# Kernel optimization log

Hardware: AMD Instinct MI355X
Metric: run time of the kernel (lower is better)

Reference implementation:

```python
import jax, jax.numpy as jnp
import numpy as np

B, S, D, H, R, N, KR = 2, 2048, 1024, 16, 256, 8, 128
DH = D // H
EPS = 1e-5


def setup_inputs() -> dict:
    key = jax.random.key(0)
    ks = jax.random.split(key, 20)
    sm = lambda k, n: jax.nn.softmax(jax.random.normal(k, (B, S, n), jnp.float32), axis=-1)
    return {
        "x": jax.random.normal(ks[0], (B, S, D), jnp.float32),
        "fqk_w_Q": sm(ks[1], N),
        "fqk_w_K": sm(ks[2], N),
        "fv_w": sm(ks[3], N),
        "rqk_w_Q": sm(ks[4], N),
        "rqk_w_K": sm(ks[5], N),
        "rv_w": sm(ks[6], N),
        "feature_know_w": sm(ks[7], N),
        "restore_know_w": sm(ks[8], N),
        "f_qk": jax.random.normal(ks[9], (N, D, R), jnp.float32) * 0.02,
        "f_v": jax.random.normal(ks[10], (N, D, R), jnp.float32) * 0.02,
        "r_qk": jax.random.normal(ks[11], (N, R, D), jnp.float32) * 0.02,
        "r_v": jax.random.normal(ks[12], (N, R, D), jnp.float32) * 0.02,
        "f_know": jax.random.normal(ks[13], (N, D, KR), jnp.float32) * 0.02,
        "r_know": jax.random.normal(ks[14], (N, KR, D), jnp.float32) * 0.02,
        "W_O": jax.random.normal(ks[15], (D, D), jnp.float32) * 0.02,
        "ln1_g": jnp.ones((D,), jnp.float32),
        "ln1_b": jnp.zeros((D,), jnp.float32),
        "ln2_g": jnp.ones((D,), jnp.float32),
        "ln2_b": jnp.zeros((D,), jnp.float32),
    }


def _layernorm(x, g, b):
    m = jnp.mean(x, axis=-1, keepdims=True)
    v = jnp.mean(jnp.square(x - m), axis=-1, keepdims=True)
    return (x - m) * jax.lax.rsqrt(v + EPS) * g + b


def _feature(x, neurons, w):
    # fused form of einsum('bsd,ndr->bsnr') + einsum('bsnr,bsn->bsr')
    return jnp.einsum('bsd,bsn,ndr->bsr', x, w, neurons)


def _restore(h, neurons, w):
    # fused form of einsum('bsr,nrd->bsnd') + einsum('bsnd,bsn->bsd')
    return jnp.einsum('bsr,bsn,nrd->bsd', h, w, neurons)


def _causal_sdpa(q, k, v):
    # q,k,v: [B,H,S,DH]
    scores = jnp.einsum('bhqd,bhkd->bhqk', q, k) / jnp.sqrt(jnp.float32(DH))
    mask = jnp.tril(jnp.ones((S, S), bool))
    scores = jnp.where(mask, scores, jnp.finfo(scores.dtype).min)
    p = jax.nn.softmax(scores, axis=-1)
    return jnp.einsum('bhqk,bhkd->bhqd', p, v)


def _block(x, fqk_w_Q, fqk_w_K, fv_w, rqk_w_Q, rqk_w_K, rv_w,
           feature_know_w, restore_know_w, f_qk, f_v, r_qk, r_v,
           f_know, r_know, W_O, ln1_g, ln1_b, ln2_g, ln2_b):
    nx = _layernorm(x, ln1_g, ln1_b)
    h_q = _feature(nx, f_qk, fqk_w_Q)
    h_k = _feature(nx, f_qk, fqk_w_K)
    h_v = _feature(nx, f_v, fv_w)
    Q = _restore(h_q, r_qk, rqk_w_Q)
    K = _restore(h_k, r_qk, rqk_w_K)
    V = _restore(h_v, r_v, rv_w)
    to_heads = lambda t: t.reshape(B, S, H, DH).transpose(0, 2, 1, 3)
    attn = _causal_sdpa(to_heads(Q), to_heads(K), to_heads(V))
    attn = attn.transpose(0, 2, 1, 3).reshape(B, S, D)
    attn_out = attn @ W_O.T  # nn.Linear(d_model,d_model,bias=False)
    x = x + attn_out
    nx2 = _layernorm(x, ln2_g, ln2_b)
    h = _feature(nx2, f_know, feature_know_w)
    know_out = _restore(h, r_know, restore_know_w)
    return x + know_out


def reference(x, fqk_w_Q, fqk_w_K, fv_w, rqk_w_Q, rqk_w_K, rv_w,
              feature_know_w, restore_know_w, f_qk, f_v, r_qk, r_v,
              f_know, r_know, W_O, ln1_g, ln1_b, ln2_g, ln2_b):
    return _block(x, fqk_w_Q, fqk_w_K, fv_w, rqk_w_Q, rqk_w_K, rv_w,
                  feature_know_w, restore_know_w, f_qk, f_v, r_qk, r_v,
                  f_know, r_know, W_O, ln1_g, ln1_b, ln2_g, ln2_b)
```

## Files before the change

### kernel.cpp

```cpp
#include <hip/hip_runtime.h>
#include <hip/hip_bf16.h>


typedef __bf16 bf16_t;
typedef __bf16 bf16x4 __attribute__((ext_vector_type(4)));
typedef __bf16 bf16x8 __attribute__((ext_vector_type(8)));
typedef float f32x4 __attribute__((ext_vector_type(4)));

#define B_DIM 2
#define S_LEN 2048
#define D_DIM 1024
#define H_NUM 16
#define DH 64
#define N_NEU 8
#define R_DIM 256
#define KR_DIM 128
#define ROWS (B_DIM * S_LEN)

static __device__ __forceinline__ void gl_lds16(const void* g, void* l)
{
    __builtin_amdgcn_global_load_lds(
        (__attribute__((address_space(1))) void*)(g),
        (__attribute__((address_space(3))) void*)(l), 16, 0, 0);
}
// ... 78 lines not shown

__global__ __launch_bounds__(256)
void ln2x_kernel(const float* __restrict__ x, const bf16_t* __restrict__ P0,
                 const bf16_t* __restrict__ P1, const float* __restrict__ g,
                 const float* __restrict__ beta, float* __restrict__ outf,
                 bf16_t* __restrict__ outn)
{
    __shared__ float red[4];
    const int row = blockIdx.x;
    const int tid = threadIdx.x;
    const size_t base = (size_t)row * D_DIM + tid * 4;
    float4 v  = *(const float4*)&x[base];
    bf16x4 p0 = *(const bf16x4*)&P0[base];
    bf16x4 p1 = *(const bf16x4*)&P1[base];
    v.x += (float)p0[0] + (float)p1[0];
    v.y += (float)p0[1] + (float)p1[1];
    v.z += (float)p0[2] + (float)p1[2];
    v.w += (float)p0[3] + (float)p1[3];
    *(float4*)&outf[base] = v;

    float s = v.x + v.y + v.z + v.w;
#pragma unroll
    for (int o = 32; o; o >>= 1) s += __shfl_down(s, o);
    if ((tid & 63) == 0) red[tid >> 6] = s;
    __syncthreads();
    float mean = (red[0] + red[1] + red[2] + red[3]) * (1.f / D_DIM);
    __syncthreads();

    float dx = v.x - mean, dy = v.y - mean, dz = v.z - mean, dw = v.w - mean;
    float q = dx * dx + dy * dy + dz * dz + dw * dw;
#pragma unroll
    for (int o = 32; o; o >>= 1) q += __shfl_down(q, o);
    if ((tid & 63) == 0) red[tid >> 6] = q;
    __syncthreads();
    float var = (red[0] + red[1] + red[2] + red[3]) * (1.f / D_DIM);
    float rstd = rsqrtf(var + 1e-5f);

    float4 gv = *(const float4*)&g[tid * 4];
    float4 bv = *(const float4*)&beta[tid * 4];
    bf16_t* op = outn + base;
    op[0] = (bf16_t)(dx * rstd * gv.x + bv.x);
    op[1] = (bf16_t)(dy * rstd * gv.y + bv.y);
    op[2] = (bf16_t)(dz * rstd * gv.z + bv.z);
    op[3] = (bf16_t)(dw * rstd * gv.w + bv.w);
}

__global__ __launch_bounds__(256)
void wsf_kernel(const bf16_t* __restrict__ y,
                const float* __restrict__ wfQ, const float* __restrict__ wrQ,
                const float* __restrict__ wfK, const float* __restrict__ wrK,
                const float* __restrict__ wfV, const float* __restrict__ wrV,
                bf16_t* __restrict__ sq, bf16_t* __restrict__ sk, bf16_t* __restrict__ sv)
{
    const int r = threadIdx.x;
    const int row = blockIdx.x;
    const bf16_t* yrow = y + (size_t)row * 4096;
    const float* fQ = wfQ + row * N_NEU;
    const float* fK = wfK + row * N_NEU;
    const float* fV = wfV + row * N_NEU;
    float aQ = 0.f, aK = 0.f, aV = 0.f;
#pragma unroll
    for (int n = 0; n < N_NEU; n++) {
        float yq = (float)yrow[n * R_DIM + r];
        float yv = (float)yrow[2048 + n * R_DIM + r];
        aQ += fQ[n] * yq;
        aK += fK[n] * yq;
        aV += fV[n] * yv;
    }
    const float* rQ = wrQ + row * N_NEU;
    const float* rK = wrK + row * N_NEU;
    const float* rV = wrV + row * N_NEU;
    const size_t rb = (size_t)row * 2048;
#pragma unroll
    for (int n = 0; n < N_NEU; n++) {
        sq[rb + n * R_DIM + r] = (bf16_t)(rQ[n] * aQ);
        sk[rb + n * R_DIM + r] = (bf16_t)(rK[n] * aK);
        sv[rb + n * R_DIM + r] = (bf16_t)(rV[n] * aV);
    }
}

__global__ __launch_bounds__(256)
void ws2_kernel(const bf16_t* __restrict__ P0, const bf16_t* __restrict__ P1,
                const float* __restrict__ wf, const float* __restrict__ wr,
                bf16_t* __restrict__ sout)
{
    const int lr = threadIdx.x >> 7;
    const int r  = threadIdx.x & 127;
    const int row = blockIdx.x * 2 + lr;
    const size_t rb = (size_t)row * (N_NEU * KR_DIM);
    const float* wfp = wf + row * N_NEU;
    const float* wrp = wr + row * N_NEU;
    float acc = 0.f;
#pragma unroll
    for (int n = 0; n < N_NEU; n++) {
        size_t i = rb + n * KR_DIM + r;
        acc += wfp[n] * ((float)P0[i] + (float)P1[i]);
    }
    bf16_t* srow = sout + rb;
#pragma unroll
    for (int n = 0; n < N_NEU; n++) srow[n * KR_DIM + r] = (bf16_t)(wrp[n] * acc);
}

template<int EPI>
__global__ __launch_bounds__(512, 2)
void gemm256_kernel(const bf16_t* __restrict__ A, const bf16_t* __restrict__ Bt,
                    const bf16_t* __restrict__ Bt2, int splitMy,
                    void* Cout, int M, int N, int K)
{
    __shared__ bf16_t As[3][256][32];
    __shared__ bf16_t Bs[3][128][32];
    const int tid = threadIdx.x;
    const int l = tid & 63, w = tid >> 6;
    const int wr = w >> 1, wc = w & 1;

    const int nbxy = gridDim.x * gridDim.y;
    int bid = blockIdx.y * gridDim.x + blockIdx.x;
    if ((nbxy & 7) == 0) bid = (bid & 7) * (nbxy >> 3) + (bid >> 3);
    const int bx = bid % gridDim.x, by = bid / gridDim.x;

    const int m0 = by * 256, n0 = bx * 128;
    const bf16_t* Bsel = (by < splitMy) ? Bt : Bt2;

    int kbeg = 0, kend = K;
    if constexpr (EPI == 2) { const int half = K >> 1; kbeg = blockIdx.z * half; kend = kbeg + half; }

    const int strow  = w * 16 + (l >> 2);
    const int scelem = ((((l & 3) * 16) ^ ((strow & 6) << 3)) >> 1);
    const bf16_t* Ag0 = A    + (size_t)(m0 + strow) * K + scelem;
    const bf16_t* Ag1 = A    + (size_t)(m0 + strow + 128) * K + scelem;
    const bf16_t* Bg0 = Bsel + (size_t)(n0 + strow) * K + scelem;

    auto stage = [&](int buf, int k0) {
        char* dA = (char*)&As[buf][0][0] + w * 1024;
        char* dB = (char*)&Bs[buf][0][0] + w * 1024;
        gl_lds16(Ag0 + k0, dA);
        gl_lds16(Ag1 + k0, dA + 8192);
        gl_lds16(Bg0 + k0, dB);
    };

    f32x4 acc[4][4];
    const f32x4 zero = {0.f, 0.f, 0.f, 0.f};
#pragma unroll
    for (int i = 0; i < 4; i++)
#pragma unroll
        for (int j = 0; j < 4; j++) acc[i][j] = zero;

    const int fr  = l & 15;
    const int fkb = (l >> 4) * 16;

    stage(0, kbeg);
    stage(1, kbeg + 32);

    const int nK = (kend - kbeg) >> 5;
// ... 21 lines not shown
            bv[i] = *(const bf16x8*)(Bb + rowB * 64 + (fkb ^ ((rowB & 6) << 3)));
        }

        if (it + 2 < nK) stage((it + 2) % 3, kbeg + (it + 2) * 32);

        __builtin_amdgcn_s_setprio(1);
#pragma unroll
        for (int mi = 0; mi < 4; mi++)
#pragma unroll
            for (int ni = 0; ni < 4; ni++)
                acc[mi][ni] = __builtin_amdgcn_mfma_f32_16x16x32_bf16(af[mi], bv[ni], acc[mi][ni], 0, 0, 0);
        __builtin_amdgcn_s_setprio(0);
    }

    const int orow = (l >> 4) * 4;
    const int ocol = l & 15;
#pragma unroll
    for (int mi = 0; mi < 4; mi++)
#pragma unroll
        for (int ni = 0; ni < 4; ni++)
#pragma unroll
            for (int j = 0; j < 4; j++) {
                int row = m0 + wr * 64 + mi * 16 + orow + j;
                int col = n0 + wc * 64 + ni * 16 + ocol;
                size_t idx = (size_t)row * N + col;
                if constexpr (EPI == 0) {
                    ((bf16_t*)Cout)[idx] = (bf16_t)acc[mi][ni][j];
                } else {
                    ((bf16_t*)Cout)[(size_t)blockIdx.z * M * N + idx] = (bf16_t)acc[mi][ni][j];
                }
            }
}

template<int EPI>
__global__ __launch_bounds__(256)
void gemm_kernel(const bf16_t* __restrict__ A, const bf16_t* __restrict__ Bt,
                 const bf16_t* __restrict__ Bt2, int splitMy,
                 void* Cout, const float* resid, int M, int N, int K)
{
    __shared__ bf16_t As[3][128][32];
    __shared__ bf16_t Bs[3][128][32];
    const int tid = threadIdx.x;
    const int l = tid & 63, w = tid >> 6;
    const int wr = w >> 1, wc = w & 1;

    const int nbxy = gridDim.x * gridDim.y;
    int bid = blockIdx.y * gridDim.x + blockIdx.x;
    if ((nbxy & 7) == 0) bid = (bid & 7) * (nbxy >> 3) + (bid >> 3);
    const int bx = bid % gridDim.x, by = bid / gridDim.x;

    const int m0 = by * 128, n0 = bx * 128;
    const bf16_t* Bsel = (by < splitMy) ? Bt : Bt2;

    int kbeg = 0, kend = K;

    const int srow = l >> 2;
    const int scolswz = (((l & 3) * 16) ^ ((srow & 6) << 3)) >> 1;
    const bf16_t* Ag0 = A    + (size_t)(m0 + w * 32 + srow) * K + scolswz;
    const bf16_t* Ag1 = Ag0 + (size_t)16 * K;
    const bf16_t* Bg0 = Bsel + (size_t)(n0 + w * 32 + srow) * K + scolswz;
    const bf16_t* Bg1 = Bg0 + (size_t)16 * K;

    auto stage = [&](int buf, int k0) {
        char* Asb = (char*)&As[buf][0][0] + w * 2048;
        char* Bsb = (char*)&Bs[buf][0][0] + w * 2048;
        gl_lds16(Ag0 + k0, Asb);
        gl_lds16(Ag1 + k0, Asb + 1024);
        gl_lds16(Bg0 + k0, Bsb);
        gl_lds16(Bg1 + k0, Bsb + 1024);
    };

    f32x4 acc[4][4];
    const f32x4 zero = {0.f, 0.f, 0.f, 0.f};
#pragma unroll
    for (int i = 0; i < 4; i++)
#pragma unroll
        for (int j = 0; j < 4; j++) acc[i][j] = zero;

    const int fr = l & 15;
    const int fkb = (l >> 4) * 16;

    stage(0, kbeg);
    stage(1, kbeg + 32);

    const int nK = (kend - kbeg) >> 5;
    for (int it = 0; it < nK; ++it) {
        if (it + 1 < nK) {
            asm volatile("s_waitcnt vmcnt(4)" ::: "memory");
        } else {
            asm volatile("s_waitcnt vmcnt(0)" ::: "memory");
        }
        __builtin_amdgcn_s_barrier();
        __builtin_amdgcn_sched_barrier(0);

        const int cur = it % 3;
        const char* Ab = (const char*)&As[cur][0][0];
        const char* Bb = (const char*)&Bs[cur][0][0];
        bf16x8 af[4], bv[4];
#pragma unroll
        for (int i = 0; i < 4; i++) {
            const int rowA = wr * 64 + i * 16 + fr;
            af[i] = *(const bf16x8*)(Ab + rowA * 64 + (fkb ^ ((rowA & 6) << 3)));
        }
#pragma unroll
        for (int i = 0; i < 4; i++) {
            const int rowB = wc * 64 + i * 16 + fr;
            bv[i] = *(const bf16x8*)(Bb + rowB * 64 + (fkb ^ ((rowB & 6) << 3)));
        }

        if (it + 2 < nK) stage((it + 2) % 3, kbeg + (it + 2) * 32);

        __builtin_amdgcn_s_setprio(1);
#pragma unroll
        for (int mi = 0; mi < 4; mi++)
#pragma unroll
            for (int ni = 0; ni < 4; ni++)
                acc[mi][ni] = __builtin_amdgcn_mfma_f32_16x16x32_bf16(af[mi], bv[ni], acc[mi][ni], 0, 0, 0);
        __builtin_amdgcn_s_setprio(0);
    }

    const int orow = (l >> 4) * 4;
    const int ocol = l & 15;
#pragma unroll
    for (int mi = 0; mi < 4; mi++)
#pragma unroll
        for (int ni = 0; ni < 4; ni++)
#pragma unroll
            for (int j = 0; j < 4; j++) {
                int row = m0 + wr * 64 + mi * 16 + orow + j;
                int col = n0 + wc * 64 + ni * 16 + ocol;
                size_t idx = (size_t)row * N + col;
                ((float*)Cout)[idx] = acc[mi][ni][j] + resid[idx];
            }
}

__global__ __launch_bounds__(256)
void fa_kernel(const bf16_t* __restrict__ Q, const bf16_t* __restrict__ K,
               const bf16_t* __restrict__ Vt, bf16_t* __restrict__ O)
{
    __shared__ bf16_t Ks[128][72];
    __shared__ bf16_t Vs[64][136];
    __shared__ bf16_t Ps[4][16][136];

    const int tid = threadIdx.x;
    const int l = tid & 63, w = tid >> 6;

    const int bid  = blockIdx.x;
    const int xcd  = bid & 7;
    const int slot = bid >> 3;
    const int head = slot & 3;
    const int jq   = slot >> 2;
    const int bh   = xcd * 4 + head;
    const int b = bh >> 4, h = bh & 15;

    const bf16_t* Qp = Q + (size_t)b * S_LEN * D_DIM + h * DH;
    const bf16_t* Kp = K + (size_t)b * S_LEN * D_DIM + h * DH;
    const bf16_t* Vp = Vt + (size_t)b * D_DIM * S_LEN + (size_t)h * DH * S_LEN;

    const int fr = l & 15, fg = l >> 4, fk = fg * 8;
    const int srow = tid >> 2;
    const int scol = (tid & 3) * 16;
    const bf16_t* Kst = Kp + (size_t)srow * D_DIM + scol;
    const bf16_t* Vst = Vp + (size_t)srow * S_LEN + scol;

    bf16x8 ones8;
#pragma unroll
    for (int i = 0; i < 8; i++) ones8[i] = (bf16_t)1.f;

    const f32x4 zero = {0.f, 0.f, 0.f, 0.f};
    const float C_LOG2 = 0.125f * 1.44269504f;

    for (int pass = 0; pass < 2; ++pass) {
        const int qb = pass ? jq : (31 - jq);
        const int q0 = qb * 64;
        const int nt = (qb >> 1) + 1;

        bf16x8 qf[2];
#pragma unroll
        for (int ks = 0; ks < 2; ks++)
            qf[ks] = *(const bf16x8*)(Qp + (size_t)(q0 + w * 16 + fr) * D_DIM + ks * 32 + fk);

        f32x4 o[4];
        f32x4 la = zero;
        float m_r[4];
#pragma unroll
        for (int j = 0; j < 4; j++) { o[j] = zero; m_r[j] = -1e30f; }

        uint4 kva = *(const uint4*)(Kst);
        uint4 kvb = *(const uint4*)(Kst + 8);
        uint4 kvc = *(const uint4*)(Kst + (size_t)64 * D_DIM);
        uint4 kvd = *(const uint4*)(Kst + (size_t)64 * D_DIM + 8);
        uint4 vva = *(const uint4*)(Vst);
        uint4 vvb = *(const uint4*)(Vst + 8);
        uint4 vvc = *(const uint4*)(Vst + 64);
        uint4 vvd = *(const uint4*)(Vst + 72);

        for (int t = 0; t < nt; t++) {
            const int k0 = t * 128;
            __syncthreads();
            *(uint4*)&Ks[srow][scol]          = kva;
            *(uint4*)&Ks[srow][scol + 8]      = kvb;
            *(uint4*)&Ks[64 + srow][scol]     = kvc;
            *(uint4*)&Ks[64 + srow][scol + 8] = kvd;
            *(uint4*)&Vs[srow][scol]          = vva;
            *(uint4*)&Vs[srow][scol + 8]      = vvb;
            *(uint4*)&Vs[srow][64 + scol]     = vvc;
            *(uint4*)&Vs[srow][64 + scol + 8] = vvd;
            __syncthreads();

            if (t + 1 < nt) {
                const int kn = k0 + 128;
                kva = *(const uint4*)(Kst + (size_t)kn * D_DIM);
                kvb = *(const uint4*)(Kst + (size_t)kn * D_DIM + 8);
                kvc = *(const uint4*)(Kst + (size_t)(kn + 64) * D_DIM);
                kvd = *(const uint4*)(Kst + (size_t)(kn + 64) * D_DIM + 8);
                vva = *(const uint4*)(Vst + kn);
                vvb = *(const uint4*)(Vst + kn + 8);
                vvc = *(const uint4*)(Vst + kn + 64);
                vvd = *(const uint4*)(Vst + kn + 72);
            }

            f32x4 sc[2][4];
#pragma unroll
            for (int s2 = 0; s2 < 2; s2++)
#pragma unroll
                for (int ni = 0; ni < 4; ni++) sc[s2][ni] = zero;
            __builtin_amdgcn_s_setprio(1);
#pragma unroll
            for (int ks = 0; ks < 2; ks++) {
#pragma unroll
                for (int s2 = 0; s2 < 2; s2++)
#pragma unroll
                    for (int ni = 0; ni < 4; ni++) {
                        bf16x8 kf = *(const bf16x8*)&Ks[s2 * 64 + ni * 16 + fr][ks * 32 + fk];
                        sc[s2][ni] = __builtin_amdgcn_mfma_f32_16x16x32_bf16(qf[ks], kf, sc[s2][ni], 0, 0, 0);
                    }
            }
            __builtin_amdgcn_s_setprio(0);

            float p[2][4][4];
            if (t == nt - 1) {
#pragma unroll
                for (int s2 = 0; s2 < 2; s2++)
#pragma unroll
                    for (int ni = 0; ni < 4; ni++) {
                        const int key = k0 + s2 * 64 + ni * 16 + fr;
#pragma unroll
                        for (int j = 0; j < 4; j++) {
                            const int qg = q0 + w * 16 + fg * 4 + j;
                            p[s2][ni][j] = (key <= qg) ? sc[s2][ni][j] * C_LOG2 : -1e30f;
                        }
                    }
            } else {
#pragma unroll
                for (int s2 = 0; s2 < 2; s2++)
#pragma unroll
                    for (int ni = 0; ni < 4; ni++)
#pragma unroll
                        for (int j = 0; j < 4; j++)
                            p[s2][ni][j] = sc[s2][ni][j] * C_LOG2;
            }

#pragma unroll
            for (int j = 0; j < 4; j++) {
                float rmax = p[0][0][j];
#pragma unroll
                for (int s2 = 0; s2 < 2; s2++)
#pragma unroll
                    for (int ni = 0; ni < 4; ni++) rmax = fmaxf(rmax, p[s2][ni][j]);
#pragma unroll
                for (int d = 1; d < 16; d <<= 1) rmax = fmaxf(rmax, __shfl_xor(rmax, d));
                if (rmax > m_r[j] + 8.f) {
                    float scale = exp2f(m_r[j] - rmax);
                    la[j] *= scale;
#pragma unroll
                    for (int nc = 0; nc < 4; nc++) o[nc][j] *= scale;
                    m_r[j] = rmax;
                }
#pragma unroll
                for (int s2 = 0; s2 < 2; s2++)
#pragma unroll
                    for (int ni = 0; ni < 4; ni++)
                        p[s2][ni][j] = exp2f(p[s2][ni][j] - m_r[j]);
            }

#pragma unroll
            for (int s2 = 0; s2 < 2; s2++)
#pragma unroll
                for (int ni = 0; ni < 4; ni++)
#pragma unroll
                    for (int j = 0; j < 4; j++)
                        Ps[w][fg * 4 + j][s2 * 64 + ni * 16 + fr] = (bf16_t)p[s2][ni][j];

            __builtin_amdgcn_s_setprio(1);
#pragma unroll
            for (int ks = 0; ks < 4; ks++) {
                bf16x8 pa = *(const bf16x8*)&Ps[w][fr][ks * 32 + fk];
                la = __builtin_amdgcn_mfma_f32_16x16x32_bf16(pa, ones8, la, 0, 0, 0);
#pragma unroll
                for (int nc = 0; nc < 4; nc++) {
                    bf16x8 vf = *(const bf16x8*)&Vs[nc * 16 + fr][ks * 32 + fk];
                    o[nc] = __builtin_amdgcn_mfma_f32_16x16x32_bf16(pa, vf, o[nc], 0, 0, 0);
                }
            }
            __builtin_amdgcn_s_setprio(0);
        }

#pragma unroll
        for (int j = 0; j < 4; j++) {
            const float inv = 1.f / la[j];
            const int q = q0 + w * 16 + fg * 4 + j;
            bf16_t* op = O + (size_t)(b * S_LEN + q) * D_DIM + h * DH;
#pragma unroll
            for (int nc = 0; nc < 4; nc++)
                op[nc * 16 + fr] = (bf16_t)(o[nc][j] * inv);
        }
    }
}

extern "C" void kernel_launch(void* const* d_in, const int* in_sizes, int n_in,
                              void* d_out, int out_size, void* d_ws, size_t ws_size,
                              hipStream_t stream)
{
    const float* x      = (const float*)d_in[0];
    const float* fqk_wQ = (const float*)d_in[1];
    const float* fqk_wK = (const float*)d_in[2];
    const float* fv_w   = (const float*)d_in[3];
    const float* rqk_wQ = (const float*)d_in[4];
    const float* rqk_wK = (const float*)d_in[5];
    const float* rv_w   = (const float*)d_in[6];
    const float* fkn_w  = (const float*)d_in[7];
    const float* rkn_w  = (const float*)d_in[8];
    const float* f_qk   = (const float*)d_in[9];
    const float* f_v    = (const float*)d_in[10];
    const float* r_qk   = (const float*)d_in[11];
    const float* r_v    = (const float*)d_in[12];
    const float* f_know = (const float*)d_in[13];
    const float* r_know = (const float*)d_in[14];
    const float* W_O    = (const float*)d_in[15];
    const float* ln1g   = (const float*)d_in[16];
    const float* ln1b   = (const float*)d_in[17];
    const float* ln2g   = (const float*)d_in[18];
    const float* ln2b   = (const float*)d_in[19];
    float* out_f = (float*)d_out;
    (void)ws_size; (void)in_sizes; (void)n_in; (void)out_size;

    char* ws = (char*)d_ws;
    const size_t MB = 1024 * 1024;
    bf16_t* rqkT   = (bf16_t*)(ws + 0 * MB);
    bf16_t* rvT    = (bf16_t*)(ws + 4 * MB);
    bf16_t* rknT   = (bf16_t*)(ws + 8 * MB);
    bf16_t* woB    = (bf16_t*)(ws + 10 * MB);
    bf16_t* fknT   = (bf16_t*)(ws + 12 * MB);
    bf16_t* buf_nx = (bf16_t*)(ws + 14 * MB);
    bf16_t* buf_y  = (bf16_t*)(ws + 22 * MB);
    char*   buf_s  = ws + 54 * MB;
    bf16_t* fqkT   = (bf16_t*)(buf_s);
    bf16_t* fvT    = (bf16_t*)(buf_s + 4 * MB);
    bf16_t* s_q    = (bf16_t*)(buf_s);
    bf16_t* s_k    = (bf16_t*)(buf_s) + (size_t)4096 * 2048;
    bf16_t* s_v    = (bf16_t*)(buf_s) + (size_t)8192 * 2048;
    bf16_t* attn   = (bf16_t*)(buf_s);
    bf16_t* P0     = (bf16_t*)(buf_s + 16 * MB);
    bf16_t* P0k    = (bf16_t*)(buf_s);
    bf16_t* sk2    = (bf16_t*)(buf_s + 32 * MB);
    bf16_t* Qb     = buf_y;
    bf16_t* Kb     = buf_y + (size_t)4096 * 1024;
    bf16_t* Vb     = buf_y + (size_t)8192 * 1024;
    bf16_t* Vt     = buf_nx;

    const dim3 blk256(256), blk512(512), blkT(32, 8);

    tcast_kernel<<<dim3(R_DIM / 32, D_DIM / 32, N_NEU), blkT, 0, stream>>>(f_qk, fqkT, D_DIM, R_DIM);
    tcast_kernel<<<dim3(R_DIM / 32, D_DIM / 32, N_NEU), blkT, 0, stream>>>(f_v, fvT, D_DIM, R_DIM);
    tcast_kernel<<<dim3(KR_DIM / 32, D_DIM / 32, N_NEU), blkT, 0, stream>>>(f_know, fknT, D_DIM, KR_DIM);
    tcast_kernel<<<dim3(D_DIM / 32, 2048 / 32, 1), blkT, 0, stream>>>(r_qk, rqkT, 2048, D_DIM);
    tcast_kernel<<<dim3(D_DIM / 32, 2048 / 32, 1), blkT, 0, stream>>>(r_v, rvT, 2048, D_DIM);
    tcast_kernel<<<dim3(D_DIM / 32, 1024 / 32, 1), blkT, 0, stream>>>(r_know, rknT, 1024, D_DIM);
    cast_kernel<<<dim3(1024 * 1024 / 4 / 256), blk256, 0, stream>>>(W_O, woB, 1024 * 1024 / 4);

    ln_kernel<<<dim3(ROWS), blk256, 0, stream>>>(x, ln1g, ln1b, buf_nx);

    gemm256_kernel<0><<<dim3(32, 16), blk512, 0, stream>>>(buf_nx, fqkT, fqkT, 1 << 30, buf_y, 4096, 4096, 1024);

    wsf_kernel<<<dim3(ROWS), blk256, 0, stream>>>(buf_y, fqk_wQ, rqk_wQ, fqk_wK, rqk_wK, fv_w, rv_w, s_q, s_k, s_v);

    gemm256_kernel<0><<<dim3(8, 48), blk512, 0, stream>>>((bf16_t*)buf_s, rqkT, rvT, 32, buf_y, 12288, 1024, 2048);

    tbf_kernel<<<dim3(D_DIM / 32, S_LEN / 32, B_DIM), blkT, 0, stream>>>(Vb, Vt, S_LEN, D_DIM);

    fa_kernel<<<dim3(512), blk256, 0, stream>>>(Qb, Kb, Vt, attn);

    gemm256_kernel<2><<<dim3(8, 16, 2), blk512, 0, stream>>>(attn, woB, woB, 1 << 30, P0, 4096, 1024, 1024);

    ln2x_kernel<<<dim3(ROWS), blk256, 0, stream>>>(x, P0, P0 + (size_t)4096 * 1024, ln2g, ln2b, out_f, buf_nx);

    gemm256_kernel<2><<<dim3(8, 16, 2), blk512, 0, stream>>>(buf_nx, fknT, fknT, 1 << 30, P0k, 4096, 1024, 1024);

    ws2_kernel<<<dim3(ROWS / 2), blk256, 0, stream>>>(P0k, P0k + (size_t)4096 * 1024, fkn_w, rkn_w, sk2);

    gemm_kernel<1><<<dim3(8, 32), blk256, 0, stream>>>(sk2, rknT, rknT, 1 << 30, d_out, out_f, 4096, 1024, 1024);
}
```

Measured before the change: 290.7 us.

## Vectorize gating kernels and split flash attention into one q-block per workgroup

The wsf and ws2 gating kernels now give each thread 8 contiguous bf16 elements with 128-bit loads and stores, handling several rows per block. This cuts per-element memory instructions and the number of tiny blocks. The flash-attention kernel no longer pairs two q-blocks per workgroup; it launches 1024 workgroups, each taking one q-block in a zig-zag order so that heavy and light causal tiles interleave across the grid. That gives finer parallelism and load balance, at the cost of relying on the hardware scheduler to even out the causal imbalance.

```diff
diff --git a/kernel.cpp b/kernel.cpp
--- a/kernel.cpp
+++ b/kernel.cpp
@@ -154,30 +154,45 @@
                 const float* __restrict__ wfV, const float* __restrict__ wrV,
                 bf16_t* __restrict__ sq, bf16_t* __restrict__ sk, bf16_t* __restrict__ sv)
 {
-    const int r = threadIdx.x;
-    const int row = blockIdx.x;
+    const int lr = threadIdx.x >> 5;
+    const int rc = (threadIdx.x & 31) * 8;
+    const int row = blockIdx.x * 8 + lr;
     const bf16_t* yrow = y + (size_t)row * 4096;
     const float* fQ = wfQ + row * N_NEU;
     const float* fK = wfK + row * N_NEU;
     const float* fV = wfV + row * N_NEU;
-    float aQ = 0.f, aK = 0.f, aV = 0.f;
+
+    float aQ[8], aK[8], aV[8];
+#pragma unroll
+    for (int i = 0; i < 8; i++) { aQ[i] = 0.f; aK[i] = 0.f; aV[i] = 0.f; }
 #pragma unroll
     for (int n = 0; n < N_NEU; n++) {
-        float yq = (float)yrow[n * R_DIM + r];
-        float yv = (float)yrow[2048 + n * R_DIM + r];
-        aQ += fQ[n] * yq;
-        aK += fK[n] * yq;
-        aV += fV[n] * yv;
+        bf16x8 vq = *(const bf16x8*)(yrow + n * R_DIM + rc);
+        bf16x8 vv = *(const bf16x8*)(yrow + 2048 + n * R_DIM + rc);
+        const float cQ = fQ[n], cK = fK[n], cV = fV[n];
+#pragma unroll
+        for (int i = 0; i < 8; i++) {
+            float q = (float)vq[i], v = (float)vv[i];
+            aQ[i] += cQ * q; aK[i] += cK * q; aV[i] += cV * v;
+        }
     }
     const float* rQ = wrQ + row * N_NEU;
     const float* rK = wrK + row * N_NEU;
     const float* rV = wrV + row * N_NEU;
-    const size_t rb = (size_t)row * 2048;
+    const size_t rb = (size_t)row * 2048 + rc;
 #pragma unroll
     for (int n = 0; n < N_NEU; n++) {
-        sq[rb + n * R_DIM + r] = (bf16_t)(rQ[n] * aQ);
-        sk[rb + n * R_DIM + r] = (bf16_t)(rK[n] * aK);
-        sv[rb + n * R_DIM + r] = (bf16_t)(rV[n] * aV);
+        bf16x8 oq, ok, ov;
+        const float cQ = rQ[n], cK = rK[n], cV = rV[n];
+#pragma unroll
+        for (int i = 0; i < 8; i++) {
+            oq[i] = (bf16_t)(cQ * aQ[i]);
+            ok[i] = (bf16_t)(cK * aK[i]);
+            ov[i] = (bf16_t)(cV * aV[i]);
+        }
+        *(bf16x8*)(sq + rb + n * R_DIM) = oq;
+        *(bf16x8*)(sk + rb + n * R_DIM) = ok;
+        *(bf16x8*)(sv + rb + n * R_DIM) = ov;
     }
 }
 
@@ -186,21 +201,32 @@
                 const float* __restrict__ wf, const float* __restrict__ wr,
                 bf16_t* __restrict__ sout)
 {
-    const int lr = threadIdx.x >> 7;
-    const int r  = threadIdx.x & 127;
-    const int row = blockIdx.x * 2 + lr;
-    const size_t rb = (size_t)row * (N_NEU * KR_DIM);
+    const int lr = threadIdx.x >> 4;
+    const int rc = (threadIdx.x & 15) * 8;
+    const int row = blockIdx.x * 16 + lr;
+    const size_t rb = (size_t)row * (N_NEU * KR_DIM) + rc;
     const float* wfp = wf + row * N_NEU;
     const float* wrp = wr + row * N_NEU;
-    float acc = 0.f;
+
+    float acc[8];
+#pragma unroll
+    for (int i = 0; i < 8; i++) acc[i] = 0.f;
 #pragma unroll
     for (int n = 0; n < N_NEU; n++) {
-        size_t i = rb + n * KR_DIM + r;
-        acc += wfp[n] * ((float)P0[i] + (float)P1[i]);
-    }
-    bf16_t* srow = sout + rb;
-#pragma unroll
-    for (int n = 0; n < N_NEU; n++) srow[n * KR_DIM + r] = (bf16_t)(wrp[n] * acc);
+        bf16x8 p0 = *(const bf16x8*)(P0 + rb + n * KR_DIM);
+        bf16x8 p1 = *(const bf16x8*)(P1 + rb + n * KR_DIM);
+        const float c = wfp[n];
+#pragma unroll
+        for (int i = 0; i < 8; i++) acc[i] += c * ((float)p0[i] + (float)p1[i]);
+    }
+#pragma unroll
+    for (int n = 0; n < N_NEU; n++) {
+        bf16x8 o;
+        const float c = wrp[n];
+#pragma unroll
+        for (int i = 0; i < 8; i++) o[i] = (bf16_t)(c * acc[i]);
+        *(bf16x8*)(sout + rb + n * KR_DIM) = o;
+    }
 }
 
 template<int EPI>
@@ -425,9 +451,13 @@
     const int xcd  = bid & 7;
     const int slot = bid >> 3;
     const int head = slot & 3;
-    const int jq   = slot >> 2;
+    const int j5   = slot >> 2;
+    const int t5   = j5 & 7, u5 = j5 >> 3;
+    const int qb   = 8 * u5 + ((u5 & 1) ? (7 - t5) : t5);
     const int bh   = xcd * 4 + head;
     const int b = bh >> 4, h = bh & 15;
+    const int q0 = qb * 64;
+    const int nt = (qb >> 1) + 1;
 
     const bf16_t* Qp = Q + (size_t)b * S_LEN * D_DIM + h * DH;
     const bf16_t* Kp = K + (size_t)b * S_LEN * D_DIM + h * DH;
@@ -446,151 +476,145 @@
     const f32x4 zero = {0.f, 0.f, 0.f, 0.f};
     const float C_LOG2 = 0.125f * 1.44269504f;
 
-    for (int pass = 0; pass < 2; ++pass) {
-        const int qb = pass ? jq : (31 - jq);
-        const int q0 = qb * 64;
-        const int nt = (qb >> 1) + 1;
-
-        bf16x8 qf[2];
-#pragma unroll
-        for (int ks = 0; ks < 2; ks++)
-            qf[ks] = *(const bf16x8*)(Qp + (size_t)(q0 + w * 16 + fr) * D_DIM + ks * 32 + fk);
-
-        f32x4 o[4];
-        f32x4 la = zero;
-        float m_r[4];
-#pragma unroll
-        for (int j = 0; j < 4; j++) { o[j] = zero; m_r[j] = -1e30f; }
-
-        uint4 kva = *(const uint4*)(Kst);
-        uint4 kvb = *(const uint4*)(Kst + 8);
-        uint4 kvc = *(const uint4*)(Kst + (size_t)64 * D_DIM);
-        uint4 kvd = *(const uint4*)(Kst + (size_t)64 * D_DIM + 8);
-        uint4 vva = *(const uint4*)(Vst);
-        uint4 vvb = *(const uint4*)(Vst + 8);
-        uint4 vvc = *(const uint4*)(Vst + 64);
-        uint4 vvd = *(const uint4*)(Vst + 72);
-
-        for (int t = 0; t < nt; t++) {
-            const int k0 = t * 128;
-            __syncthreads();
-            *(uint4*)&Ks[srow][scol]          = kva;
-            *(uint4*)&Ks[srow][scol + 8]      = kvb;
-            *(uint4*)&Ks[64 + srow][scol]     = kvc;
-            *(uint4*)&Ks[64 + srow][scol + 8] = kvd;
-            *(uint4*)&Vs[srow][scol]          = vva;
-            *(uint4*)&Vs[srow][scol + 8]      = vvb;
-            *(uint4*)&Vs[srow][64 + scol]     = vvc;
-            *(uint4*)&Vs[srow][64 + scol + 8] = vvd;
-            __syncthreads();
-
-            if (t + 1 < nt) {
-                const int kn = k0 + 128;
-                kva = *(const uint4*)(Kst + (size_t)kn * D_DIM);
-                kvb = *(const uint4*)(Kst + (size_t)kn * D_DIM + 8);
-                kvc = *(const uint4*)(Kst + (size_t)(kn + 64) * D_DIM);
-                kvd = *(const uint4*)(Kst + (size_t)(kn + 64) * D_DIM + 8);
-                vva = *(const uint4*)(Vst + kn);
-                vvb = *(const uint4*)(Vst + kn + 8);
-                vvc = *(const uint4*)(Vst + kn + 64);
-                vvd = *(const uint4*)(Vst + kn + 72);
+    bf16x8 qf[2];
+#pragma unroll
+    for (int ks = 0; ks < 2; ks++)
+        qf[ks] = *(const bf16x8*)(Qp + (size_t)(q0 + w * 16 + fr) * D_DIM + ks * 32 + fk);
+
+    f32x4 o[4];
+    f32x4 la = zero;
+    float m_r[4];
+#pragma unroll
+    for (int j = 0; j < 4; j++) { o[j] = zero; m_r[j] = -1e30f; }
+
+    uint4 kva = *(const uint4*)(Kst);
+    uint4 kvb = *(const uint4*)(Kst + 8);
+    uint4 kvc = *(const uint4*)(Kst + (size_t)64 * D_DIM);
+    uint4 kvd = *(const uint4*)(Kst + (size_t)64 * D_DIM + 8);
+    uint4 vva = *(const uint4*)(Vst);
+    uint4 vvb = *(const uint4*)(Vst + 8);
+    uint4 vvc = *(const uint4*)(Vst + 64);
+    uint4 vvd = *(const uint4*)(Vst + 72);
+
+    for (int t = 0; t < nt; t++) {
+        const int k0 = t * 128;
+        __syncthreads();
+        *(uint4*)&Ks[srow][scol]          = kva;
+        *(uint4*)&Ks[srow][scol + 8]      = kvb;
+        *(uint4*)&Ks[64 + srow][scol]     = kvc;
+        *(uint4*)&Ks[64 + srow][scol + 8] = kvd;
+        *(uint4*)&Vs[srow][scol]          = vva;
+        *(uint4*)&Vs[srow][scol + 8]      = vvb;
+        *(uint4*)&Vs[srow][64 + scol]     = vvc;
+        *(uint4*)&Vs[srow][64 + scol + 8] = vvd;
+        __syncthreads();
+
+        if (t + 1 < nt) {
+            const int kn = k0 + 128;
+            kva = *(const uint4*)(Kst + (size_t)kn * D_DIM);
+            kvb = *(const uint4*)(Kst + (size_t)kn * D_DIM + 8);
+            kvc = *(const uint4*)(Kst + (size_t)(kn + 64) * D_DIM);
+            kvd = *(const uint4*)(Kst + (size_t)(kn + 64) * D_DIM + 8);
+            vva = *(const uint4*)(Vst + kn);
+            vvb = *(const uint4*)(Vst + kn + 8);
+            vvc = *(const uint4*)(Vst + kn + 64);
+            vvd = *(const uint4*)(Vst + kn + 72);
+        }
+
+        f32x4 sc[2][4];
+#pragma unroll
+        for (int s2 = 0; s2 < 2; s2++)
+#pragma unroll
+            for (int ni = 0; ni < 4; ni++) sc[s2][ni] = zero;
+        __builtin_amdgcn_s_setprio(1);
+#pragma unroll
+        for (int ks = 0; ks < 2; ks++) {
+#pragma unroll
+            for (int s2 = 0; s2 < 2; s2++)
+#pragma unroll
+                for (int ni = 0; ni < 4; ni++) {
+                    bf16x8 kf = *(const bf16x8*)&Ks[s2 * 64 + ni * 16 + fr][ks * 32 + fk];
+                    sc[s2][ni] = __builtin_amdgcn_mfma_f32_16x16x32_bf16(qf[ks], kf, sc[s2][ni], 0, 0, 0);
+                }
+        }
+        __builtin_amdgcn_s_setprio(0);
+
+        float p[2][4][4];
+        if (t == nt - 1) {
+#pragma unroll
+            for (int s2 = 0; s2 < 2; s2++)
+#pragma unroll
+                for (int ni = 0; ni < 4; ni++) {
+                    const int key = k0 + s2 * 64 + ni * 16 + fr;
+#pragma unroll
+                    for (int j = 0; j < 4; j++) {
+                        const int qg = q0 + w * 16 + fg * 4 + j;
+                        p[s2][ni][j] = (key <= qg) ? sc[s2][ni][j] * C_LOG2 : -1e30f;
+                    }
+                }
+        } else {
+#pragma unroll
+            for (int s2 = 0; s2 < 2; s2++)
+#pragma unroll
+                for (int ni = 0; ni < 4; ni++)
+#pragma unroll
+                    for (int j = 0; j < 4; j++)
+                        p[s2][ni][j] = sc[s2][ni][j] * C_LOG2;
+        }
+
+#pragma unroll
+        for (int j = 0; j < 4; j++) {
+            float rmax = p[0][0][j];
+#pragma unroll
+            for (int s2 = 0; s2 < 2; s2++)
+#pragma unroll
+                for (int ni = 0; ni < 4; ni++) rmax = fmaxf(rmax, p[s2][ni][j]);
+#pragma unroll
+            for (int d = 1; d < 16; d <<= 1) rmax = fmaxf(rmax, __shfl_xor(rmax, d));
+            if (rmax > m_r[j] + 8.f) {
+                float scale = exp2f(m_r[j] - rmax);
+                la[j] *= scale;
+#pragma unroll
+                for (int nc = 0; nc < 4; nc++) o[nc][j] *= scale;
+                m_r[j] = rmax;
             }
-
-            f32x4 sc[2][4];
 #pragma unroll
             for (int s2 = 0; s2 < 2; s2++)
 #pragma unroll
-                for (int ni = 0; ni < 4; ni++) sc[s2][ni] = zero;
-            __builtin_amdgcn_s_setprio(1);
-#pragma unroll
-            for (int ks = 0; ks < 2; ks++) {
-#pragma unroll
-                for (int s2 = 0; s2 < 2; s2++)
-#pragma unroll
-                    for (int ni = 0; ni < 4; ni++) {
-                        bf16x8 kf = *(const bf16x8*)&Ks[s2 * 64 + ni * 16 + fr][ks * 32 + fk];
-                        sc[s2][ni] = __builtin_amdgcn_mfma_f32_16x16x32_bf16(qf[ks], kf, sc[s2][ni], 0, 0, 0);
-                    }
+                for (int ni = 0; ni < 4; ni++)
+                    p[s2][ni][j] = exp2f(p[s2][ni][j] - m_r[j]);
+        }
+
+#pragma unroll
+        for (int s2 = 0; s2 < 2; s2++)
+#pragma unroll
+            for (int ni = 0; ni < 4; ni++)
+#pragma unroll
+                for (int j = 0; j < 4; j++)
+                    Ps[w][fg * 4 + j][s2 * 64 + ni * 16 + fr] = (bf16_t)p[s2][ni][j];
+
+        __builtin_amdgcn_s_setprio(1);
+#pragma unroll
+        for (int ks = 0; ks < 4; ks++) {
+            bf16x8 pa = *(const bf16x8*)&Ps[w][fr][ks * 32 + fk];
+            la = __builtin_amdgcn_mfma_f32_16x16x32_bf16(pa, ones8, la, 0, 0, 0);
+#pragma unroll
+            for (int nc = 0; nc < 4; nc++) {
+                bf16x8 vf = *(const bf16x8*)&Vs[nc * 16 + fr][ks * 32 + fk];
+                o[nc] = __builtin_amdgcn_mfma_f32_16x16x32_bf16(pa, vf, o[nc], 0, 0, 0);
             }
-            __builtin_amdgcn_s_setprio(0);
-
-            float p[2][4][4];
-            if (t == nt - 1) {
-#pragma unroll
-                for (int s2 = 0; s2 < 2; s2++)
-#pragma unroll
-                    for (int ni = 0; ni < 4; ni++) {
-                        const int key = k0 + s2 * 64 + ni * 16 + fr;
-#pragma unroll
-                        for (int j = 0; j < 4; j++) {
-                            const int qg = q0 + w * 16 + fg * 4 + j;
-                            p[s2][ni][j] = (key <= qg) ? sc[s2][ni][j] * C_LOG2 : -1e30f;
-                        }
-                    }
-            } else {
-#pragma unroll
-                for (int s2 = 0; s2 < 2; s2++)
-#pragma unroll
-                    for (int ni = 0; ni < 4; ni++)
-#pragma unroll
-                        for (int j = 0; j < 4; j++)
-                            p[s2][ni][j] = sc[s2][ni][j] * C_LOG2;
-            }
-
-#pragma unroll
-            for (int j = 0; j < 4; j++) {
-                float rmax = p[0][0][j];
-#pragma unroll
-                for (int s2 = 0; s2 < 2; s2++)
-#pragma unroll
-                    for (int ni = 0; ni < 4; ni++) rmax = fmaxf(rmax, p[s2][ni][j]);
-#pragma unroll
-                for (int d = 1; d < 16; d <<= 1) rmax = fmaxf(rmax, __shfl_xor(rmax, d));
-                if (rmax > m_r[j] + 8.f) {
-                    float scale = exp2f(m_r[j] - rmax);
-                    la[j] *= scale;
-#pragma unroll
-                    for (int nc = 0; nc < 4; nc++) o[nc][j] *= scale;
-                    m_r[j] = rmax;
-                }
-#pragma unroll
-                for (int s2 = 0; s2 < 2; s2++)
-#pragma unroll
-                    for (int ni = 0; ni < 4; ni++)
-                        p[s2][ni][j] = exp2f(p[s2][ni][j] - m_r[j]);
-            }
-
-#pragma unroll
-            for (int s2 = 0; s2 < 2; s2++)
-#pragma unroll
-                for (int ni = 0; ni < 4; ni++)
-#pragma unroll
-                    for (int j = 0; j < 4; j++)
-                        Ps[w][fg * 4 + j][s2 * 64 + ni * 16 + fr] = (bf16_t)p[s2][ni][j];
-
-            __builtin_amdgcn_s_setprio(1);
-#pragma unroll
-            for (int ks = 0; ks < 4; ks++) {
-                bf16x8 pa = *(const bf16x8*)&Ps[w][fr][ks * 32 + fk];
-                la = __builtin_amdgcn_mfma_f32_16x16x32_bf16(pa, ones8, la, 0, 0, 0);
-#pragma unroll
-                for (int nc = 0; nc < 4; nc++) {
-                    bf16x8 vf = *(const bf16x8*)&Vs[nc * 16 + fr][ks * 32 + fk];
-                    o[nc] = __builtin_amdgcn_mfma_f32_16x16x32_bf16(pa, vf, o[nc], 0, 0, 0);
-                }
-            }
-            __builtin_amdgcn_s_setprio(0);
-        }
-
-#pragma unroll
-        for (int j = 0; j < 4; j++) {
-            const float inv = 1.f / la[j];
-            const int q = q0 + w * 16 + fg * 4 + j;
-            bf16_t* op = O + (size_t)(b * S_LEN + q) * D_DIM + h * DH;
-#pragma unroll
-            for (int nc = 0; nc < 4; nc++)
-                op[nc * 16 + fr] = (bf16_t)(o[nc][j] * inv);
-        }
+        }
+        __builtin_amdgcn_s_setprio(0);
+    }
+
+#pragma unroll
+    for (int j = 0; j < 4; j++) {
+        const float inv = 1.f / la[j];
+        const int q = q0 + w * 16 + fg * 4 + j;
+        bf16_t* op = O + (size_t)(b * S_LEN + q) * D_DIM + h * DH;
+#pragma unroll
+        for (int nc = 0; nc < 4; nc++)
+            op[nc * 16 + fr] = (bf16_t)(o[nc][j] * inv);
     }
 }
 
@@ -659,13 +683,13 @@
 
     gemm256_kernel<0><<<dim3(32, 16), blk512, 0, stream>>>(buf_nx, fqkT, fqkT, 1 << 30, buf_y, 4096, 4096, 1024);
 
-    wsf_kernel<<<dim3(ROWS), blk256, 0, stream>>>(buf_y, fqk_wQ, rqk_wQ, fqk_wK, rqk_wK, fv_w, rv_w, s_q, s_k, s_v);
+    wsf_kernel<<<dim3(ROWS / 8), blk256, 0, stream>>>(buf_y, fqk_wQ, rqk_wQ, fqk_wK, rqk_wK, fv_w, rv_w, s_q, s_k, s_v);
 
     gemm256_kernel<0><<<dim3(8, 48), blk512, 0, stream>>>((bf16_t*)buf_s, rqkT, rvT, 32, buf_y, 12288, 1024, 2048);
 
     tbf_kernel<<<dim3(D_DIM / 32, S_LEN / 32, B_DIM), blkT, 0, stream>>>(Vb, Vt, S_LEN, D_DIM);
 
-    fa_kernel<<<dim3(512), blk256, 0, stream>>>(Qb, Kb, Vt, attn);
+    fa_kernel<<<dim3(1024), blk256, 0, stream>>>(Qb, Kb, Vt, attn);
 
     gemm256_kernel<2><<<dim3(8, 16, 2), blk512, 0, stream>>>(attn, woB, woB, 1 << 30, P0, 4096, 1024, 1024);
 
@@ -673,7 +697,7 @@
 
     gemm256_kernel<2><<<dim3(8, 16, 2), blk512, 0, stream>>>(buf_nx, fknT, fknT, 1 << 30, P0k, 4096, 1024, 1024);
 
-    ws2_kernel<<<dim3(ROWS / 2), blk256, 0, stream>>>(P0k, P0k + (size_t)4096 * 1024, fkn_w, rkn_w, sk2);
+    ws2_kernel<<<dim3(ROWS / 16), blk256, 0, stream>>>(P0k, P0k + (size_t)4096 * 1024, fkn_w, rkn_w, sk2);
 
     gemm_kernel<1><<<dim3(8, 32), blk256, 0, stream>>>(sk2, rknT, rknT, 1 << 30, d_out, out_f, 4096, 1024, 1024);
 }
```

New measurement: 298.0 us. 2.5% more time.

## Restructure flash attention to one query tile per block with double-buffered 64-key tiles

Applied to the files above, without the earlier changes.

The attention kernel now launches one block per 64-query tile instead of pairing two tiles per block. It walks 64-key tiles with double-buffered, XOR-swizzled LDS and a serpentine ordering of query blocks to balance causal work, and sets launch bounds for higher occupancy. The restore GEMM also switches from the 256-tile kernel to the 128-tile gemm_kernel, which gains a bf16 epilogue, so twice as many blocks run. The goal is more parallelism and fewer LDS bank conflicts. The cost is more key/value reloads across blocks and smaller MFMA work per sync.

```diff
diff --git a/kernel.cpp b/kernel.cpp
--- a/kernel.cpp
+++ b/kernel.cpp
@@ -328,7 +328,7 @@
     const int m0 = by * 128, n0 = bx * 128;
     const bf16_t* Bsel = (by < splitMy) ? Bt : Bt2;
 
-    int kbeg = 0, kend = K;
+    const int kbeg = 0, kend = K;
 
     const int srow = l >> 2;
     const int scolswz = (((l & 3) * 16) ^ ((srow & 6) << 3)) >> 1;
@@ -406,17 +406,21 @@
                 int row = m0 + wr * 64 + mi * 16 + orow + j;
                 int col = n0 + wc * 64 + ni * 16 + ocol;
                 size_t idx = (size_t)row * N + col;
-                ((float*)Cout)[idx] = acc[mi][ni][j] + resid[idx];
+                if constexpr (EPI == 0) {
+                    ((bf16_t*)Cout)[idx] = (bf16_t)acc[mi][ni][j];
+                } else {
+                    ((float*)Cout)[idx] = acc[mi][ni][j] + resid[idx];
+                }
             }
 }
 
-__global__ __launch_bounds__(256)
+__global__ __launch_bounds__(256, 4)
 void fa_kernel(const bf16_t* __restrict__ Q, const bf16_t* __restrict__ K,
                const bf16_t* __restrict__ Vt, bf16_t* __restrict__ O)
 {
-    __shared__ bf16_t Ks[128][72];
-    __shared__ bf16_t Vs[64][136];
-    __shared__ bf16_t Ps[4][16][136];
+    __shared__ bf16_t Ks[2][64][64];
+    __shared__ bf16_t Vs[2][64][64];
+    __shared__ bf16_t Ps[4][16][64];
 
     const int tid = threadIdx.x;
     const int l = tid & 63, w = tid >> 6;
@@ -425,9 +429,13 @@
     const int xcd  = bid & 7;
     const int slot = bid >> 3;
     const int head = slot & 3;
-    const int jq   = slot >> 2;
+    const int j5   = slot >> 2;
+    const int t5   = j5 & 7, u5 = j5 >> 3;
+    const int qb   = 8 * u5 + ((u5 & 1) ? (7 - t5) : t5);
     const int bh   = xcd * 4 + head;
     const int b = bh >> 4, h = bh & 15;
+    const int q0 = qb * 64;
+    const int nt = qb + 1;
 
     const bf16_t* Qp = Q + (size_t)b * S_LEN * D_DIM + h * DH;
     const bf16_t* Kp = K + (size_t)b * S_LEN * D_DIM + h * DH;
@@ -435,9 +443,10 @@
 
     const int fr = l & 15, fg = l >> 4, fk = fg * 8;
     const int srow = tid >> 2;
-    const int scol = (tid & 3) * 16;
-    const bf16_t* Kst = Kp + (size_t)srow * D_DIM + scol;
-    const bf16_t* Vst = Vp + (size_t)srow * S_LEN + scol;
+    const int scel = (tid & 3) * 16;
+    const int swz  = (srow & 7) << 4;
+    const bf16_t* Kst = Kp + (size_t)srow * D_DIM + scel;
+    const bf16_t* Vst = Vp + (size_t)srow * S_LEN + scel;
 
     bf16x8 ones8;
 #pragma unroll
@@ -446,151 +455,145 @@
     const f32x4 zero = {0.f, 0.f, 0.f, 0.f};
     const float C_LOG2 = 0.125f * 1.44269504f;
 
-    for (int pass = 0; pass < 2; ++pass) {
-        const int qb = pass ? jq : (31 - jq);
-        const int q0 = qb * 64;
-        const int nt = (qb >> 1) + 1;
-
-        bf16x8 qf[2];
-#pragma unroll
-        for (int ks = 0; ks < 2; ks++)
-            qf[ks] = *(const bf16x8*)(Qp + (size_t)(q0 + w * 16 + fr) * D_DIM + ks * 32 + fk);
-
-        f32x4 o[4];
-        f32x4 la = zero;
-        float m_r[4];
-#pragma unroll
-        for (int j = 0; j < 4; j++) { o[j] = zero; m_r[j] = -1e30f; }
-
-        uint4 kva = *(const uint4*)(Kst);
-        uint4 kvb = *(const uint4*)(Kst + 8);
-        uint4 kvc = *(const uint4*)(Kst + (size_t)64 * D_DIM);
-        uint4 kvd = *(const uint4*)(Kst + (size_t)64 * D_DIM + 8);
-        uint4 vva = *(const uint4*)(Vst);
-        uint4 vvb = *(const uint4*)(Vst + 8);
-        uint4 vvc = *(const uint4*)(Vst + 64);
-        uint4 vvd = *(const uint4*)(Vst + 72);
-
-        for (int t = 0; t < nt; t++) {
-            const int k0 = t * 128;
-            __syncthreads();
-            *(uint4*)&Ks[srow][scol]          = kva;
-            *(uint4*)&Ks[srow][scol + 8]      = kvb;
-            *(uint4*)&Ks[64 + srow][scol]     = kvc;
-            *(uint4*)&Ks[64 + srow][scol + 8] = kvd;
-            *(uint4*)&Vs[srow][scol]          = vva;
-            *(uint4*)&Vs[srow][scol + 8]      = vvb;
-            *(uint4*)&Vs[srow][64 + scol]     = vvc;
-            *(uint4*)&Vs[srow][64 + scol + 8] = vvd;
-            __syncthreads();
-
-            if (t + 1 < nt) {
-                const int kn = k0 + 128;
-                kva = *(const uint4*)(Kst + (size_t)kn * D_DIM);
-                kvb = *(const uint4*)(Kst + (size_t)kn * D_DIM + 8);
-                kvc = *(const uint4*)(Kst + (size_t)(kn + 64) * D_DIM);
-                kvd = *(const uint4*)(Kst + (size_t)(kn + 64) * D_DIM + 8);
-                vva = *(const uint4*)(Vst + kn);
-                vvb = *(const uint4*)(Vst + kn + 8);
-                vvc = *(const uint4*)(Vst + kn + 64);
-                vvd = *(const uint4*)(Vst + kn + 72);
+    bf16x8 qf[2];
+#pragma unroll
+    for (int ks = 0; ks < 2; ks++)
+        qf[ks] = *(const bf16x8*)(Qp + (size_t)(q0 + w * 16 + fr) * D_DIM + ks * 32 + fk);
+
+    f32x4 o[4];
+    f32x4 la = zero;
+    float m_r[4];
+#pragma unroll
+    for (int j = 0; j < 4; j++) { o[j] = zero; m_r[j] = -1e30f; }
+
+    uint4 ka = *(const uint4*)(Kst);
+    uint4 kb = *(const uint4*)(Kst + 8);
+    uint4 va = *(const uint4*)(Vst);
+    uint4 vb = *(const uint4*)(Vst + 8);
+    {
+        char* kd = (char*)&Ks[0][srow][0];
+        char* vd = (char*)&Vs[0][srow][0];
+        *(uint4*)(kd + ((scel * 2)      ^ swz)) = ka;
+        *(uint4*)(kd + ((scel * 2 + 16) ^ swz)) = kb;
+        *(uint4*)(vd + ((scel * 2)      ^ swz)) = va;
+        *(uint4*)(vd + ((scel * 2 + 16) ^ swz)) = vb;
+    }
+    if (nt > 1) {
+        ka = *(const uint4*)(Kst + (size_t)64 * D_DIM);
+        kb = *(const uint4*)(Kst + (size_t)64 * D_DIM + 8);
+        va = *(const uint4*)(Vst + 64);
+        vb = *(const uint4*)(Vst + 64 + 8);
+    }
+    __syncthreads();
+
+    for (int t = 0; t < nt; t++) {
+        const int cur = t & 1;
+
+        if (t + 1 < nt) {
+            char* kd = (char*)&Ks[cur ^ 1][srow][0];
+            char* vd = (char*)&Vs[cur ^ 1][srow][0];
+            *(uint4*)(kd + ((scel * 2)      ^ swz)) = ka;
+            *(uint4*)(kd + ((scel * 2 + 16) ^ swz)) = kb;
+            *(uint4*)(vd + ((scel * 2)      ^ swz)) = va;
+            *(uint4*)(vd + ((scel * 2 + 16) ^ swz)) = vb;
+        }
+        if (t + 2 < nt) {
+            const size_t kn = (size_t)(t + 2) * 64;
+            ka = *(const uint4*)(Kst + kn * D_DIM);
+            kb = *(const uint4*)(Kst + kn * D_DIM + 8);
+            va = *(const uint4*)(Vst + kn);
+            vb = *(const uint4*)(Vst + kn + 8);
+        }
+
+        const int k0 = t * 64;
+        f32x4 sc[4];
+#pragma unroll
+        for (int ni = 0; ni < 4; ni++) sc[ni] = zero;
+        __builtin_amdgcn_s_setprio(1);
+#pragma unroll
+        for (int ks = 0; ks < 2; ks++) {
+#pragma unroll
+            for (int ni = 0; ni < 4; ni++) {
+                const int row = ni * 16 + fr;
+                bf16x8 kf = *(const bf16x8*)((const char*)&Ks[cur][row][0]
+                              + ((ks * 64 + fg * 16) ^ ((fr & 7) << 4)));
+                sc[ni] = __builtin_amdgcn_mfma_f32_16x16x32_bf16(qf[ks], kf, sc[ni], 0, 0, 0);
             }
-
-            f32x4 sc[2][4];
-#pragma unroll
-            for (int s2 = 0; s2 < 2; s2++)
-#pragma unroll
-                for (int ni = 0; ni < 4; ni++) sc[s2][ni] = zero;
-            __builtin_amdgcn_s_setprio(1);
-#pragma unroll
-            for (int ks = 0; ks < 2; ks++) {
-#pragma unroll
-                for (int s2 = 0; s2 < 2; s2++)
-#pragma unroll
-                    for (int ni = 0; ni < 4; ni++) {
-                        bf16x8 kf = *(const bf16x8*)&Ks[s2 * 64 + ni * 16 + fr][ks * 32 + fk];
-                        sc[s2][ni] = __builtin_amdgcn_mfma_f32_16x16x32_bf16(qf[ks], kf, sc[s2][ni], 0, 0, 0);
-                    }
-            }
-            __builtin_amdgcn_s_setprio(0);
-
-            float p[2][4][4];
-            if (t == nt - 1) {
-#pragma unroll
-                for (int s2 = 0; s2 < 2; s2++)
-#pragma unroll
-                    for (int ni = 0; ni < 4; ni++) {
-                        const int key = k0 + s2 * 64 + ni * 16 + fr;
-#pragma unroll
-                        for (int j = 0; j < 4; j++) {
-                            const int qg = q0 + w * 16 + fg * 4 + j;
-                            p[s2][ni][j] = (key <= qg) ? sc[s2][ni][j] * C_LOG2 : -1e30f;
-                        }
-                    }
-            } else {
-#pragma unroll
-                for (int s2 = 0; s2 < 2; s2++)
-#pragma unroll
-                    for (int ni = 0; ni < 4; ni++)
-#pragma unroll
-                        for (int j = 0; j < 4; j++)
-                            p[s2][ni][j] = sc[s2][ni][j] * C_LOG2;
-            }
-
-#pragma unroll
-            for (int j = 0; j < 4; j++) {
-                float rmax = p[0][0][j];
-#pragma unroll
-                for (int s2 = 0; s2 < 2; s2++)
-#pragma unroll
-                    for (int ni = 0; ni < 4; ni++) rmax = fmaxf(rmax, p[s2][ni][j]);
-#pragma unroll
-                for (int d = 1; d < 16; d <<= 1) rmax = fmaxf(rmax, __shfl_xor(rmax, d));
-                if (rmax > m_r[j] + 8.f) {
-                    float scale = exp2f(m_r[j] - rmax);
-                    la[j] *= scale;
-#pragma unroll
-                    for (int nc = 0; nc < 4; nc++) o[nc][j] *= scale;
-                    m_r[j] = rmax;
-                }
-#pragma unroll
-                for (int s2 = 0; s2 < 2; s2++)
-#pragma unroll
-                    for (int ni = 0; ni < 4; ni++)
-                        p[s2][ni][j] = exp2f(p[s2][ni][j] - m_r[j]);
-            }
-
-#pragma unroll
-            for (int s2 = 0; s2 < 2; s2++)
-#pragma unroll
-                for (int ni = 0; ni < 4; ni++)
-#pragma unroll
-                    for (int j = 0; j < 4; j++)
-                        Ps[w][fg * 4 + j][s2 * 64 + ni * 16 + fr] = (bf16_t)p[s2][ni][j];
-
-            __builtin_amdgcn_s_setprio(1);
-#pragma unroll
-            for (int ks = 0; ks < 4; ks++) {
-                bf16x8 pa = *(const bf16x8*)&Ps[w][fr][ks * 32 + fk];
-                la = __builtin_amdgcn_mfma_f32_16x16x32_bf16(pa, ones8, la, 0, 0, 0);
-#pragma unroll
-                for (int nc = 0; nc < 4; nc++) {
-                    bf16x8 vf = *(const bf16x8*)&Vs[nc * 16 + fr][ks * 32 + fk];
-                    o[nc] = __builtin_amdgcn_mfma_f32_16x16x32_bf16(pa, vf, o[nc], 0, 0, 0);
+        }
+        __builtin_amdgcn_s_setprio(0);
+
+        float p[4][4];
+        if (t == qb) {
+#pragma unroll
+            for (int ni = 0; ni < 4; ni++) {
+                const int key = k0 + ni * 16 + fr;
+#pragma unroll
+                for (int j = 0; j < 4; j++) {
+                    const int qg = q0 + w * 16 + fg * 4 + j;
+                    p[ni][j] = (key <= qg) ? sc[ni][j] * C_LOG2 : -1e30f;
                 }
             }
-            __builtin_amdgcn_s_setprio(0);
+        } else {
+#pragma unroll
+            for (int ni = 0; ni < 4; ni++)
+#pragma unroll
+                for (int j = 0; j < 4; j++)
+                    p[ni][j] = sc[ni][j] * C_LOG2;
         }
 
 #pragma unroll
         for (int j = 0; j < 4; j++) {
-            const float inv = 1.f / la[j];
-            const int q = q0 + w * 16 + fg * 4 + j;
-            bf16_t* op = O + (size_t)(b * S_LEN + q) * D_DIM + h * DH;
-#pragma unroll
-            for (int nc = 0; nc < 4; nc++)
-                op[nc * 16 + fr] = (bf16_t)(o[nc][j] * inv);
-        }
+            float rmax = fmaxf(fmaxf(p[0][j], p[1][j]), fmaxf(p[2][j], p[3][j]));
+#pragma unroll
+            for (int d = 1; d < 16; d <<= 1) rmax = fmaxf(rmax, __shfl_xor(rmax, d));
+            if (rmax > m_r[j] + 8.f) {
+                float scale = exp2f(m_r[j] - rmax);
+                la[j] *= scale;
+#pragma unroll
+                for (int nc = 0; nc < 4; nc++) o[nc][j] *= scale;
+                m_r[j] = rmax;
+            }
+#pragma unroll
+            for (int ni = 0; ni < 4; ni++)
+                p[ni][j] = exp2f(p[ni][j] - m_r[j]);
+        }
+
+#pragma unroll
+        for (int ni = 0; ni < 4; ni++)
+#pragma unroll
+            for (int j = 0; j < 4; j++) {
+                const int qrow = fg * 4 + j;
+                char* pd = (char*)&Ps[w][qrow][0];
+                *(bf16_t*)(pd + (((ni * 16 + fr) * 2) ^ ((qrow & 7) << 4))) = (bf16_t)p[ni][j];
+            }
+
+        __builtin_amdgcn_s_setprio(1);
+#pragma unroll
+        for (int ks = 0; ks < 2; ks++) {
+            bf16x8 pa = *(const bf16x8*)((const char*)&Ps[w][fr][0]
+                          + ((ks * 64 + fg * 16) ^ ((fr & 7) << 4)));
+            la = __builtin_amdgcn_mfma_f32_16x16x32_bf16(pa, ones8, la, 0, 0, 0);
+#pragma unroll
+            for (int nc = 0; nc < 4; nc++) {
+                const int row = nc * 16 + fr;
+                bf16x8 vf = *(const bf16x8*)((const char*)&Vs[cur][row][0]
+                              + ((ks * 64 + fg * 16) ^ ((fr & 7) << 4)));
+                o[nc] = __builtin_amdgcn_mfma_f32_16x16x32_bf16(pa, vf, o[nc], 0, 0, 0);
+            }
+        }
+        __builtin_amdgcn_s_setprio(0);
+
+        __syncthreads();
+    }
+
+#pragma unroll
+    for (int j = 0; j < 4; j++) {
+        const float inv = 1.f / la[j];
+        const int q = q0 + w * 16 + fg * 4 + j;
+        bf16_t* op = O + (size_t)(b * S_LEN + q) * D_DIM + h * DH;
+#pragma unroll
+        for (int nc = 0; nc < 4; nc++)
+            op[nc * 16 + fr] = (bf16_t)(o[nc][j] * inv);
     }
 }
 
@@ -661,11 +664,11 @@
 
     wsf_kernel<<<dim3(ROWS), blk256, 0, stream>>>(buf_y, fqk_wQ, rqk_wQ, fqk_wK, rqk_wK, fv_w, rv_w, s_q, s_k, s_v);
 
-    gemm256_kernel<0><<<dim3(8, 48), blk512, 0, stream>>>((bf16_t*)buf_s, rqkT, rvT, 32, buf_y, 12288, 1024, 2048);
+    gemm_kernel<0><<<dim3(8, 96), blk256, 0, stream>>>((bf16_t*)buf_s, rqkT, rvT, 64, buf_y, nullptr, 12288, 1024, 2048);
 
     tbf_kernel<<<dim3(D_DIM / 32, S_LEN / 32, B_DIM), blkT, 0, stream>>>(Vb, Vt, S_LEN, D_DIM);
 
-    fa_kernel<<<dim3(512), blk256, 0, stream>>>(Qb, Kb, Vt, attn);
+    fa_kernel<<<dim3(1024), blk256, 0, stream>>>(Qb, Kb, Vt, attn);
 
     gemm256_kernel<2><<<dim3(8, 16, 2), blk512, 0, stream>>>(attn, woB, woB, 1 << 30, P0, 4096, 1024, 1024);
 
```

New measurement: 315.3 us. +8.4%, slower.
